# Performance work log

Hardware: AMD Instinct MI355X
Metric: run time of the kernel (lower is better)

## Reference

```python
import jax, jax.numpy as jnp
import numpy as np

B, S, D = 8, 1024, 768
H, DK, DV = 12, 64, 64


def setup_inputs() -> dict:
    key = jax.random.key(0)
    ks = jax.random.split(key, 8)
    s_in = 1.0 / np.sqrt(D)
    s_cat = 1.0 / np.sqrt(H * DV)
    return {
        "x": jax.random.normal(ks[0], (B, S, D), jnp.float32),
        "Wq": jax.random.normal(ks[1], (H, D, DK), jnp.float32) * s_in,
        "bq": jnp.zeros((H, DK), jnp.float32),
        "Wk": jax.random.normal(ks[2], (H, D, DK), jnp.float32) * s_in,
        "bk": jnp.zeros((H, DK), jnp.float32),
        "Wv": jax.random.normal(ks[3], (H, D, DV), jnp.float32) * s_in,
        "bv": jnp.zeros((H, DV), jnp.float32),
        "W0": jax.random.normal(ks[4], (H * DV, D), jnp.float32) * s_cat,
        "b0": jnp.zeros((D,), jnp.float32),
    }


def reference(x, Wq, bq, Wk, bk, Wv, bv, W0, b0):
    # Per-head projections, batched across heads (same math as the ModuleList loop).
    q = jnp.einsum("bsd,hdk->bhsk", x, Wq) + bq[None, :, None, :]  # [B,H,S,DK]
    k = jnp.einsum("bsd,hdk->bhsk", x, Wk) + bk[None, :, None, :]
    v = jnp.einsum("bsd,hdv->bhsv", x, Wv) + bv[None, :, None, :]
    scale = 1.0 / jnp.sqrt(jnp.asarray(DK, x.dtype))
    scores = jnp.einsum("bhqk,bhsk->bhqs", q, k) * scale  # [B,H,S,S]
    causal = jnp.tril(jnp.ones((S, S), bool))
    scores = jnp.where(causal[None, None], scores, jnp.asarray(-1e9, x.dtype))
    attn = jax.nn.softmax(scores, axis=-1)
    out = jnp.einsum("bhqs,bhsv->bhqv", attn, v)  # [B,H,S,DV]
    # concat heads along last dim -> [B,S,H*DV]
    out = jnp.transpose(out, (0, 2, 1, 3)).reshape(B, S, H * DV)
    # output projection (dropout is identity in eval mode / p=0)
    return out @ W0 + b0
```

## Files before the change

### kernel.cpp

```cpp
#include <hip/hip_runtime.h>


typedef __attribute__((ext_vector_type(8))) short short8;
typedef __attribute__((ext_vector_type(4))) short short4_t;
typedef __attribute__((ext_vector_type(4))) float f32x4;

#define Bsz 8
#define Ssz 1024
#define Dsz 768
#define Hsz 12
#define DKsz 64
#define KVB 128

__device__ __forceinline__ short f2bf(float f) {
    unsigned u = __float_as_uint(f);
    u = (u + 0x7fffu + ((u >> 16) & 1u)) >> 16;
    return (short)u;
}

__device__ __forceinline__ float fexp2(float x) {
    float r;
    asm("v_exp_f32 %0, %1" : "=v"(r) : "v"(x));
    return r;
}

__device__ __forceinline__ f32x4 mfma16(short8 a, short8 b, f32x4 c) {
    return __builtin_amdgcn_mfma_f32_16x16x32_bf16(a, b, c, 0, 0, 0);
}

__device__ __forceinline__ void gload16(const short* g, short* lds) {
    __builtin_amdgcn_global_load_lds(
        (const __attribute__((address_space(1))) void*)g,
        (__attribute__((address_space(3))) void*)lds, 16, 0, 0);
}

__global__ __launch_bounds__(256) void cast_x_kernel(const float* __restrict__ x,
                                                     short* __restrict__ xbf) {
    int i = (blockIdx.x * 256 + threadIdx.x) * 8;
    float4 a = *reinterpret_cast<const float4*>(&x[i]);
    float4 b = *reinterpret_cast<const float4*>(&x[i + 4]);
    short8 o;
    o[0] = f2bf(a.x); o[1] = f2bf(a.y); o[2] = f2bf(a.z); o[3] = f2bf(a.w);
    o[4] = f2bf(b.x); o[5] = f2bf(b.y); o[6] = f2bf(b.z); o[7] = f2bf(b.w);
    *reinterpret_cast<short8*>(&xbf[i]) = o;
}

__global__ __launch_bounds__(256) void pack_qkvw_kernel(const float* __restrict__ Wq,
                                                        const float* __restrict__ Wk,
                                                        const float* __restrict__ Wv,
                                                        short* __restrict__ Wt) {
    int idx = blockIdx.x * 256 + threadIdx.x;
    int n = idx / Dsz;
    int k = idx % Dsz;
    int which = n / 768;
    int hc = n - which * 768;
    int h = hc >> 6, c = hc & 63;
    const float* W = (which == 0) ? Wq : (which == 1) ? Wk : Wv;
    Wt[idx] = f2bf(W[(h * Dsz + k) * DKsz + c]);
}

__global__ __launch_bounds__(256) void pack_w0_kernel(const float* __restrict__ W0,
                                                      short* __restrict__ W0t) {
    int idx = blockIdx.x * 256 + threadIdx.x;
    int n = idx / Dsz;
    int k = idx % Dsz;
    W0t[idx] = f2bf(W0[k * Dsz + n]);
}

#define GEMM_MAIN(A_, Bt_, Kdim)                                                   \
    int tid = threadIdx.x, w = tid >> 6, l = tid & 63;                             \
    int wr = w >> 1, wc = w & 1;                                                   \
    int lr = l & 15, lg = l >> 4;                                                  \
    __shared__ short Als[2][128 * 32];                                             \
    __shared__ short Bls[2][128 * 32];                                             \
    f32x4 acc[4][4] = {};                                                          \
    auto STAGE = [&](int cb, int k0) {                                             \
        _Pragma("unroll")                                                          \
        for (int j = 0; j < 2; ++j) {                                              \
            int i = j * 256 + w * 64 + l;                                          \
            int r = i >> 2, sl = i & 3;                                            \
            gload16((A_) + r * (Kdim) + k0 + ((sl ^ (r & 3)) << 3),                \
                    &Als[cb][(j * 256 + w * 64) * 8]);                             \
            gload16((Bt_) + r * (Kdim) + k0 + ((sl ^ (r & 3)) << 3),               \
                    &Bls[cb][(j * 256 + w * 64) * 8]);                             \
        }                                                                          \
    };                                                                             \
    auto COMPUTE = [&](int cb) {                                                   \
        short8 af[4], bf[4];                                                       \
        _Pragma("unroll")                                                          \
        for (int m = 0; m < 4; ++m) {                                              \
            int row = wr * 64 + m * 16 + lr;                                       \
            af[m] = *reinterpret_cast<const short8*>(                              \
                &Als[cb][row * 32 + ((lg ^ (row & 3)) << 3)]);                     \
        }                                                                          \
        _Pragma("unroll")                                                          \
        for (int n = 0; n < 4; ++n) {                                              \
            int row = wc * 64 + n * 16 + lr;                                       \
            bf[n] = *reinterpret_cast<const short8*>(                              \
                &Bls[cb][row * 32 + ((lg ^ (row & 3)) << 3)]);                     \
        }                                                                          \
        _Pragma("unroll")                                                          \
        for (int m = 0; m < 4; ++m)                                                \
            _Pragma("unroll")                                                      \
            for (int n = 0; n < 4; ++n)                                            \
                acc[m][n] = mfma16(af[m], bf[n], acc[m][n]);                       \
    };                                                                             \
    int cur = 0;                                                                   \
    STAGE(0, 0);                                                                   \
    __syncthreads();                                                               \
    for (int k0 = 32; k0 < (Kdim); k0 += 32) {                                     \
        STAGE(cur ^ 1, k0);                                                        \
        COMPUTE(cur);                                                              \
        __syncthreads();                                                           \
        cur ^= 1;                                                                  \
    }                                                                              \
    COMPUTE(cur);

__global__ __launch_bounds__(256) void gemm_qkv_kernel(
    const short* __restrict__ A, const short* __restrict__ Bt,
    const float* __restrict__ bq, const float* __restrict__ bk,
    const float* __restrict__ bv,
    short* __restrict__ Qb, short* __restrict__ Kb, short* __restrict__ Vb) {
    int tile = (blockIdx.x & 7) * 144 + (blockIdx.x >> 3);
    int tm = tile / 18, tn = tile % 18;
    const short* Ab = A + (size_t)tm * 128 * Dsz;
    const short* Bb = Bt + (size_t)tn * 128 * Dsz;
    GEMM_MAIN(Ab, Bb, Dsz)
    int which = tn / 6;
    const float* bias = (which == 0) ? bq : (which == 1) ? bk : bv;
    int row0 = tm * 128 + wr * 64;
    int col0 = tn * 128 + wc * 64 - which * 768;
    if (which == 2) {
#pragma unroll
        for (int m = 0; m < 4; ++m)
#pragma unroll
            for (int n = 0; n < 4; ++n) {
                int s0 = row0 + m * 16 + lg * 4;
                int col = col0 + n * 16 + lr;
                int b = s0 >> 10, s = s0 & 1023;
                int h = col >> 6, c = col & 63;
                float bi = bias[h * 64 + c];
                short4_t pk;
#pragma unroll
                for (int j = 0; j < 4; ++j) pk[j] = f2bf(acc[m][n][j] + bi);
                *reinterpret_cast<short4_t*>(
                    &Vb[(((size_t)b * Hsz + h) * DKsz + c) * Ssz + s]) = pk;
            }
    } else {
        short* dst = (which == 0) ? Qb : Kb;
#pragma unroll
        for (int m = 0; m < 4; ++m)
#pragma unroll
            for (int n = 0; n < 4; ++n)
#pragma unroll
                for (int j = 0; j < 4; ++j) {
                    int row = row0 + m * 16 + lg * 4 + j;
                    int col = col0 + n * 16 + lr;
                    int b = row >> 10, s = row & 1023;
                    int h = col >> 6, c = col & 63;
                    float v = acc[m][n][j] + bias[h * 64 + c];
                    if (which == 0) v *= 0.180336884f;
                    dst[(((size_t)b * Hsz + h) * Ssz + s) * DKsz + c] = f2bf(v);
                }
    }
}

__global__ __launch_bounds__(256) void attn_kernel(const short* __restrict__ Q,
                                                   const short* __restrict__ K,
                                                   const short* __restrict__ Vt,
                                                   short* __restrict__ O) {
    int raw = blockIdx.x;
    int xcd = raw & 7, slot = raw >> 3;
    int bh  = (slot >> 4) * 8 + xcd;
    int qb  = 15 - (slot & 15);
    const short* Qh = Q + (size_t)bh * Ssz * DKsz;
    const short* Kh = K + (size_t)bh * Ssz * DKsz;
    const short* Vh = Vt + (size_t)bh * DKsz * Ssz;
    int tid = threadIdx.x, w = tid >> 6, l = tid & 63;
    int lr = l & 15, lg = l >> 4;
    __shared__ short Kls[KVB * 64];
    __shared__ short Vls[64 * KVB];
    __shared__ short Pls[4][16 * KVB];

    int qrow = qb * 64 + w * 16 + lr;
    short8 aq0 = *reinterpret_cast<const short8*>(&Qh[qrow * 64 + lg * 8]);
    short8 aq1 = *reinterpret_cast<const short8*>(&Qh[qrow * 64 + 32 + lg * 8]);

    short8 ones;
#pragma unroll
    for (int e = 0; e < 8; ++e) ones[e] = (short)0x3F80;

    f32x4 acc[4] = {};
    f32x4 accL = {};

    int nt = qb / 2 + 1;
    for (int t = 0; t < nt; ++t) {
        __syncthreads();
        const short* Ksrc = Kh + t * KVB * 64;
#pragma unroll
        for (int it = 0; it < 4; ++it) {
            int i = it * 256 + tid;
            int r = i >> 3, ps = i & 7;
            gload16(Ksrc + r * 64 + ((ps ^ (r & 7)) << 3),
                    &Kls[(it * 256 + w * 64) * 8]);
        }
#pragma unroll
        for (int it = 0; it < 4; ++it) {
            int i = it * 256 + tid;
            int r = i >> 4, ps = i & 15;
            gload16(Vh + r * Ssz + t * KVB + ((ps ^ (r & 15)) << 3),
                    &Vls[(it * 256 + w * 64) * 8]);
        }
        __syncthreads();

        f32x4 s[8] = {};
        __builtin_amdgcn_s_setprio(1);
#pragma unroll
        for (int n = 0; n < 8; ++n) {
            int kr = n * 16 + lr;
            short8 kf0 = *reinterpret_cast<const short8*>(
                &Kls[kr * 64 + ((lg ^ (kr & 7)) << 3)]);
            short8 kf1 = *reinterpret_cast<const short8*>(
                &Kls[kr * 64 + (((lg + 4) ^ (kr & 7)) << 3)]);
            s[n] = mfma16(aq0, kf0, s[n]);
            s[n] = mfma16(aq1, kf1, s[n]);
        }
        __builtin_amdgcn_s_setprio(0);

        if (t == nt - 1) {
#pragma unroll
            for (int n = 0; n < 8; ++n)
#pragma unroll
                for (int j = 0; j < 4; ++j) {
                    int kv = t * KVB + n * 16 + lr;
                    int q = qb * 64 + w * 16 + lg * 4 + j;
                    if (kv > q) s[n][j] = -1e30f;
                }
        }

#pragma unroll
        for (int n = 0; n < 8; ++n)
#pragma unroll
            for (int j = 0; j < 4; ++j) {
                float p = fexp2(s[n][j]);
                int row = lg * 4 + j;
                int col = n * 16 + lr;
                Pls[w][row * KVB + (col ^ (row << 3))] = f2bf(p);
            }

        __builtin_amdgcn_s_setprio(1);
#pragma unroll
        for (int kk = 0; kk < 4; ++kk) {
            int sl = (((kk * 4 + lg) ^ lr) << 3);
            short8 pa = *reinterpret_cast<const short8*>(&Pls[w][lr * KVB + sl]);
            accL = mfma16(pa, ones, accL);
#pragma unroll
            for (int n = 0; n < 4; ++n) {
                short8 vf = *reinterpret_cast<const short8*>(
                    &Vls[(n * 16 + lr) * KVB + sl]);
                acc[n] = mfma16(pa, vf, acc[n]);
            }
        }
        __builtin_amdgcn_s_setprio(0);
    }

    int b = bh / Hsz, h = bh % Hsz;
#pragma unroll
    for (int n = 0; n < 4; ++n)
#pragma unroll
        for (int j = 0; j < 4; ++j) {
            int q = qb * 64 + w * 16 + lg * 4 + j;
            int dv = n * 16 + lr;
            float o = acc[n][j] / accL[j];
            O[((size_t)(b * Ssz + q)) * Dsz + h * DKsz + dv] = f2bf(o);
        }
}

__global__ __launch_bounds__(256) void gemm_out_kernel(const short* __restrict__ A,
                                                       const short* __restrict__ Bt,
                                                       const float* __restrict__ b0,
                                                       float* __restrict__ out) {
    int tile = (blockIdx.x & 7) * 48 + (blockIdx.x >> 3);
    int tm = tile / 6, tn = tile % 6;
    const short* Ab = A + (size_t)tm * 128 * Dsz;
    const short* Bb = Bt + (size_t)tn * 128 * Dsz;
    GEMM_MAIN(Ab, Bb, Dsz)
    int row0 = tm * 128 + wr * 64;
    int col0 = tn * 128 + wc * 64;
#pragma unroll
    for (int m = 0; m < 4; ++m)
#pragma unroll
        for (int n = 0; n < 4; ++n)
#pragma unroll
            for (int j = 0; j < 4; ++j) {
                int row = row0 + m * 16 + lg * 4 + j;
                int col = col0 + n * 16 + lr;
                out[(size_t)row * Dsz + col] = acc[m][n][j] + b0[col];
            }
}

extern "C" void kernel_launch(void* const* d_in, const int* in_sizes, int n_in,
                              void* d_out, int out_size, void* d_ws, size_t ws_size,
                              hipStream_t stream) {
    const float* x  = (const float*)d_in[0];
    const float* Wq = (const float*)d_in[1];
    const float* bq = (const float*)d_in[2];
    const float* Wk = (const float*)d_in[3];
    const float* bk = (const float*)d_in[4];
    const float* Wv = (const float*)d_in[5];
    const float* bv = (const float*)d_in[6];
    const float* W0 = (const float*)d_in[7];
    const float* b0 = (const float*)d_in[8];
    float* out = (float*)d_out;

    const size_t N_X   = (size_t)Bsz * Ssz * Dsz;
    const size_t N_QKV = (size_t)3 * Dsz * Dsz;
    const size_t N_W0  = (size_t)Dsz * Dsz;
    const size_t N_HD  = (size_t)Bsz * Hsz * Ssz * DKsz;

    short* xbf   = (short*)d_ws;
    short* wqkvt = xbf + N_X;
    short* w0t   = wqkvt + N_QKV;
    short* Qb    = w0t + N_W0;
    short* Kb    = Qb + N_HD;
    short* Vb    = Kb + N_HD;
    short* attno = Vb + N_HD;

    cast_x_kernel<<<(int)(N_X / 2048), 256, 0, stream>>>(x, xbf);
    pack_qkvw_kernel<<<(int)(N_QKV / 256), 256, 0, stream>>>(Wq, Wk, Wv, wqkvt);
    pack_w0_kernel<<<(int)(N_W0 / 256), 256, 0, stream>>>(W0, w0t);
    gemm_qkv_kernel<<<64 * 18, 256, 0, stream>>>(xbf, wqkvt, bq, bk, bv, Qb, Kb, Vb);
    attn_kernel<<<Bsz * Hsz * 16, 256, 0, stream>>>(Qb, Kb, Vb, attno);
    gemm_out_kernel<<<64 * 6, 256, 0, stream>>>(attno, w0t, b0, out);
}
```

Baseline: 231.1 us.

## Enlarge GEMM tiles to 256 rows with 512 threads and vmcnt-based pipelining

Both projection GEMMs move from 128x128 tiles on 256 threads to 256-row tiles on 512 threads (256x256 for QKV, 256x128 for the output). The main loop is restructured to keep two stages in flight, using explicit s_waitcnt vmcnt plus raw barriers in place of __syncthreads. The aim is more operand reuse per LDS load and better overlap of global loads with MFMA work. The trade-off is fewer blocks (288 and 192 on a GPU with many CUs), which risks tail underutilization, plus higher register pressure from the larger accumulator arrays.

```diff
diff --git a/kernel.cpp b/kernel.cpp
--- a/kernel.cpp
+++ b/kernel.cpp
@@ -32,6 +32,12 @@
     __builtin_amdgcn_global_load_lds(
         (const __attribute__((address_space(1))) void*)g,
         (__attribute__((address_space(3))) void*)lds, 16, 0, 0);
+}
+
+template <int N> __device__ __forceinline__ void waitv() {
+    if constexpr (N == 4)      asm volatile("s_waitcnt vmcnt(4)" ::: "memory");
+    else if constexpr (N == 3) asm volatile("s_waitcnt vmcnt(3)" ::: "memory");
+    else                       asm volatile("s_waitcnt vmcnt(0)" ::: "memory");
 }
 
 __global__ __launch_bounds__(256) void cast_x_kernel(const float* __restrict__ x,
@@ -67,72 +73,80 @@
     W0t[idx] = f2bf(W0[k * Dsz + n]);
 }
 
-#define GEMM_MAIN(A_, Bt_, Kdim)                                                   \
+#define GEMM_MAIN256(A_, Bt_, Kdim, NF_, WAITN_)                                   \
     int tid = threadIdx.x, w = tid >> 6, l = tid & 63;                             \
-    int wr = w >> 1, wc = w & 1;                                                   \
+    int wr = w >> 2, wc = w & 3;                                                   \
     int lr = l & 15, lg = l >> 4;                                                  \
-    __shared__ short Als[2][128 * 32];                                             \
-    __shared__ short Bls[2][128 * 32];                                             \
-    f32x4 acc[4][4] = {};                                                          \
+    __shared__ short Als[2][256 * 32];                                             \
+    __shared__ short Bls[2][(NF_ * 64) * 32];                                      \
+    f32x4 acc[8][NF_] = {};                                                        \
     auto STAGE = [&](int cb, int k0) {                                             \
         _Pragma("unroll")                                                          \
-        for (int j = 0; j < 2; ++j) {                                              \
-            int i = j * 256 + w * 64 + l;                                          \
+        for (int it = 0; it < 2; ++it) {                                           \
+            int i = it * 512 + tid;                                                \
             int r = i >> 2, sl = i & 3;                                            \
             gload16((A_) + r * (Kdim) + k0 + ((sl ^ (r & 3)) << 3),                \
-                    &Als[cb][(j * 256 + w * 64) * 8]);                             \
+                    &Als[cb][(it * 512 + w * 64) * 8]);                            \
+        }                                                                          \
+        _Pragma("unroll")                                                          \
+        for (int it = 0; it < (NF_) / 2; ++it) {                                   \
+            int i = it * 512 + tid;                                                \
+            int r = i >> 2, sl = i & 3;                                            \
             gload16((Bt_) + r * (Kdim) + k0 + ((sl ^ (r & 3)) << 3),               \
-                    &Bls[cb][(j * 256 + w * 64) * 8]);                             \
+                    &Bls[cb][(it * 512 + w * 64) * 8]);                            \
         }                                                                          \
     };                                                                             \
     auto COMPUTE = [&](int cb) {                                                   \
-        short8 af[4], bf[4];                                                       \
+        short8 bf[NF_];                                                            \
         _Pragma("unroll")                                                          \
-        for (int m = 0; m < 4; ++m) {                                              \
-            int row = wr * 64 + m * 16 + lr;                                       \
-            af[m] = *reinterpret_cast<const short8*>(                              \
-                &Als[cb][row * 32 + ((lg ^ (row & 3)) << 3)]);                     \
-        }                                                                          \
-        _Pragma("unroll")                                                          \
-        for (int n = 0; n < 4; ++n) {                                              \
-            int row = wc * 64 + n * 16 + lr;                                       \
+        for (int n = 0; n < (NF_); ++n) {                                          \
+            int row = wc * ((NF_) * 16) + n * 16 + lr;                             \
             bf[n] = *reinterpret_cast<const short8*>(                              \
                 &Bls[cb][row * 32 + ((lg ^ (row & 3)) << 3)]);                     \
         }                                                                          \
         _Pragma("unroll")                                                          \
-        for (int m = 0; m < 4; ++m)                                                \
+        for (int m = 0; m < 8; ++m) {                                              \
+            int row = wr * 128 + m * 16 + lr;                                      \
+            short8 af = *reinterpret_cast<const short8*>(                          \
+                &Als[cb][row * 32 + ((lg ^ (row & 3)) << 3)]);                     \
             _Pragma("unroll")                                                      \
-            for (int n = 0; n < 4; ++n)                                            \
-                acc[m][n] = mfma16(af[m], bf[n], acc[m][n]);                       \
+            for (int n = 0; n < (NF_); ++n)                                        \
+                acc[m][n] = mfma16(af, bf[n], acc[m][n]);                          \
+        }                                                                          \
     };                                                                             \
-    int cur = 0;                                                                   \
     STAGE(0, 0);                                                                   \
-    __syncthreads();                                                               \
-    for (int k0 = 32; k0 < (Kdim); k0 += 32) {                                     \
-        STAGE(cur ^ 1, k0);                                                        \
-        COMPUTE(cur);                                                              \
-        __syncthreads();                                                           \
-        cur ^= 1;                                                                  \
+    STAGE(1, 32);                                                                  \
+    for (int k = 0; k < (Kdim) / 32 - 2; ++k) {                                    \
+        waitv<WAITN_>();                                                           \
+        __builtin_amdgcn_s_barrier();                                              \
+        COMPUTE(k & 1);                                                            \
+        __builtin_amdgcn_s_barrier();                                              \
+        STAGE(k & 1, (k + 2) * 32);                                                \
     }                                                                              \
-    COMPUTE(cur);
-
-__global__ __launch_bounds__(256) void gemm_qkv_kernel(
+    waitv<WAITN_>();                                                               \
+    __builtin_amdgcn_s_barrier();                                                  \
+    COMPUTE(((Kdim) / 32 - 2) & 1);                                                \
+    waitv<0>();                                                                    \
+    __builtin_amdgcn_s_barrier();                                                  \
+    COMPUTE(((Kdim) / 32 - 1) & 1);
+
+__global__ __launch_bounds__(512, 2) void gemm_qkv_kernel(
     const short* __restrict__ A, const short* __restrict__ Bt,
     const float* __restrict__ bq, const float* __restrict__ bk,
     const float* __restrict__ bv,
     short* __restrict__ Qb, short* __restrict__ Kb, short* __restrict__ Vb) {
-    int tile = (blockIdx.x & 7) * 144 + (blockIdx.x >> 3);
-    int tm = tile / 18, tn = tile % 18;
-    const short* Ab = A + (size_t)tm * 128 * Dsz;
-    const short* Bb = Bt + (size_t)tn * 128 * Dsz;
-    GEMM_MAIN(Ab, Bb, Dsz)
-    int which = tn / 6;
+    int tile = (blockIdx.x & 7) * 36 + (blockIdx.x >> 3);
+    int tm = tile / 9, tn = tile % 9;
+    const short* Ab = A + (size_t)tm * 256 * Dsz;
+    const short* Bb = Bt + (size_t)tn * 256 * Dsz;
+    GEMM_MAIN256(Ab, Bb, Dsz, 4, 4)
+    int which = tn / 3;
     const float* bias = (which == 0) ? bq : (which == 1) ? bk : bv;
-    int row0 = tm * 128 + wr * 64;
-    int col0 = tn * 128 + wc * 64 - which * 768;
+    int row0 = tm * 256 + wr * 128;
+    int col0 = tn * 256 + wc * 64 - which * 768;
     if (which == 2) {
 #pragma unroll
-        for (int m = 0; m < 4; ++m)
+        for (int m = 0; m < 8; ++m)
 #pragma unroll
             for (int n = 0; n < 4; ++n) {
                 int s0 = row0 + m * 16 + lg * 4;
@@ -149,7 +163,7 @@
     } else {
         short* dst = (which == 0) ? Qb : Kb;
 #pragma unroll
-        for (int m = 0; m < 4; ++m)
+        for (int m = 0; m < 8; ++m)
 #pragma unroll
             for (int n = 0; n < 4; ++n)
 #pragma unroll
@@ -276,21 +290,21 @@
         }
 }
 
-__global__ __launch_bounds__(256) void gemm_out_kernel(const short* __restrict__ A,
-                                                       const short* __restrict__ Bt,
-                                                       const float* __restrict__ b0,
-                                                       float* __restrict__ out) {
-    int tile = (blockIdx.x & 7) * 48 + (blockIdx.x >> 3);
+__global__ __launch_bounds__(512, 2) void gemm_out_kernel(const short* __restrict__ A,
+                                                          const short* __restrict__ Bt,
+                                                          const float* __restrict__ b0,
+                                                          float* __restrict__ out) {
+    int tile = (blockIdx.x & 7) * 24 + (blockIdx.x >> 3);
     int tm = tile / 6, tn = tile % 6;
-    const short* Ab = A + (size_t)tm * 128 * Dsz;
+    const short* Ab = A + (size_t)tm * 256 * Dsz;
     const short* Bb = Bt + (size_t)tn * 128 * Dsz;
-    GEMM_MAIN(Ab, Bb, Dsz)
-    int row0 = tm * 128 + wr * 64;
-    int col0 = tn * 128 + wc * 64;
-#pragma unroll
-    for (int m = 0; m < 4; ++m)
-#pragma unroll
-        for (int n = 0; n < 4; ++n)
+    GEMM_MAIN256(Ab, Bb, Dsz, 2, 3)
+    int row0 = tm * 256 + wr * 128;
+    int col0 = tn * 128 + wc * 32;
+#pragma unroll
+    for (int m = 0; m < 8; ++m)
+#pragma unroll
+        for (int n = 0; n < 2; ++n)
 #pragma unroll
             for (int j = 0; j < 4; ++j) {
                 int row = row0 + m * 16 + lg * 4 + j;
@@ -329,7 +343,7 @@
     cast_x_kernel<<<(int)(N_X / 2048), 256, 0, stream>>>(x, xbf);
     pack_qkvw_kernel<<<(int)(N_QKV / 256), 256, 0, stream>>>(Wq, Wk, Wv, wqkvt);
     pack_w0_kernel<<<(int)(N_W0 / 256), 256, 0, stream>>>(W0, w0t);
-    gemm_qkv_kernel<<<64 * 18, 256, 0, stream>>>(xbf, wqkvt, bq, bk, bv, Qb, Kb, Vb);
+    gemm_qkv_kernel<<<288, 512, 0, stream>>>(xbf, wqkvt, bq, bk, bv, Qb, Kb, Vb);
     attn_kernel<<<Bsz * Hsz * 16, 256, 0, stream>>>(Qb, Kb, Vb, attno);
-    gemm_out_kernel<<<64 * 6, 256, 0, stream>>>(attno, w0t, b0, out);
-}
+    gemm_out_kernel<<<192, 512, 0, stream>>>(attno, w0t, b0, out);
+}
```

Result: faster. 226.5 us (-2.0%).
